# Kernel tuning notes

Hardware: AMD Instinct MI355X
Metric: run time of the kernel (lower is better)

## Reference

```python
import jax, jax.numpy as jnp
import numpy as np

L, D, H, DH, WS, FF = 4, 256, 8, 32, 128, 1024
B, N = 2, 8192
SCALE = DH ** -0.5
EPS = 1e-8


def setup_inputs() -> dict:
    key = jax.random.key(0)
    ks = jax.random.split(key, 24)
    nrm = lambda k, shape, s=0.02: jax.random.normal(k, shape, dtype=jnp.float32) * s
    d = {}
    d["x_real"] = jax.random.normal(ks[0], (B, N, D), dtype=jnp.float32)
    d["x_imag"] = jax.random.normal(ks[1], (B, N, D), dtype=jnp.float32)
    # complex attention projection weights, stored [in, out] (y = x @ W)
    d["Wq_r"] = nrm(ks[2], (L, D, D)); d["Wq_i"] = nrm(ks[3], (L, D, D))
    d["Wk_r"] = nrm(ks[4], (L, D, D)); d["Wk_i"] = nrm(ks[5], (L, D, D))
    d["Wv_r"] = nrm(ks[6], (L, D, D)); d["Wv_i"] = nrm(ks[7], (L, D, D))
    d["Wo_r"] = nrm(ks[8], (L, D, D)); d["Wo_i"] = nrm(ks[9], (L, D, D))
    d["rel_bias"] = nrm(ks[10], (L, 2 * WS + 1))  # std=0.02 per nn.init.normal_
    d["norm1_scale"] = jnp.ones((L, D), jnp.float32)
    d["norm2_scale"] = jnp.ones((L, D), jnp.float32)
    # ComplexFeedForward: real nn.Linear pairs with biases
    d["W1_r"] = nrm(ks[11], (L, D, FF)); d["b1_r"] = jnp.zeros((L, FF), jnp.float32)
    d["W1_i"] = nrm(ks[12], (L, D, FF)); d["b1_i"] = jnp.zeros((L, FF), jnp.float32)
    d["W2_r"] = nrm(ks[13], (L, FF, D)); d["b2_r"] = jnp.zeros((L, D), jnp.float32)
    d["W2_i"] = nrm(ks[14], (L, FF, D)); d["b2_i"] = jnp.zeros((L, D), jnp.float32)
    return d


def _rmsnorm(xr, xi, scale):
    rms = jnp.sqrt(jnp.mean(xr * xr + xi * xi, axis=-1, keepdims=True) + EPS)
    return xr / rms * scale, xi / rms * scale


def _cmm(xr, xi, Wr, Wi):
    # (xr + i xi) @ (Wr + i Wi)
    return xr @ Wr - xi @ Wi, xr @ Wi + xi @ Wr


def _split_heads(t):  # [B,N,H*DH] -> [B,H,NW,WS,DH]
    return t.reshape(B, N // WS, WS, H, DH).transpose(0, 3, 1, 2, 4)


def _attn(xr, xi, Wq_r, Wq_i, Wk_r, Wk_i, Wv_r, Wv_i, Wo_r, Wo_i, rel_bias):
    qr, qi = _cmm(xr, xi, Wq_r, Wq_i)
    kr, ki = _cmm(xr, xi, Wk_r, Wk_i)
    vr, vi = _cmm(xr, xi, Wv_r, Wv_i)
    qr, qi, kr, ki, vr, vi = map(_split_heads, (qr, qi, kr, ki, vr, vi))
    # Re(q . conj(k)) = qr.kr + qi.ki ; windowed (N % WS == 0, no padding)
    dots = (jnp.einsum('bhwid,bhwjd->bhwij', qr, kr)
            + jnp.einsum('bhwid,bhwjd->bhwij', qi, ki)) * SCALE
    idx = (jnp.arange(WS)[None, :] - jnp.arange(WS)[:, None]).clip(-WS, WS) + WS
    dots = dots + rel_bias[idx]  # broadcast over b,h,w
    attn = jax.nn.softmax(dots, axis=-1)  # real-valued probs
    or_ = jnp.einsum('bhwij,bhwjd->bhwid', attn, vr)
    oi_ = jnp.einsum('bhwij,bhwjd->bhwid', attn, vi)
    merge = lambda t: t.transpose(0, 2, 3, 1, 4).reshape(B, N, H * DH)
    or_, oi_ = merge(or_), merge(oi_)
    return _cmm(or_, oi_, Wo_r, Wo_i)


def _ffn(xr, xi, W1_r, b1_r, W1_i, b1_i, W2_r, b2_r, W2_i, b2_i):
    # faithful: w_real(x.real) - w_imag(x.imag) etc., each linear carries its bias
    hr = (xr @ W1_r + b1_r) - (xi @ W1_i + b1_i)
    hi = (xi @ W1_r + b1_r) + (xr @ W1_i + b1_i)
    hr = jax.nn.gelu(hr, approximate=False)
    hi = jax.nn.gelu(hi, approximate=False)
    yr = (hr @ W2_r + b2_r) - (hi @ W2_i + b2_i)
    yi = (hi @ W2_r + b2_r) + (hr @ W2_i + b2_i)
    return yr, yi


def _forward(x_real, x_imag, Wq_r, Wq_i, Wk_r, Wk_i, Wv_r, Wv_i, Wo_r, Wo_i,
             rel_bias, norm1_scale, norm2_scale,
             W1_r, b1_r, W1_i, b1_i, W2_r, b2_r, W2_i, b2_i):
    xr, xi = x_real, x_imag
    for l in range(L):
        nr, ni = _rmsnorm(xr, xi, norm1_scale[l])
        ar, ai = _attn(nr, ni, Wq_r[l], Wq_i[l], Wk_r[l], Wk_i[l],
                       Wv_r[l], Wv_i[l], Wo_r[l], Wo_i[l], rel_bias[l])
        xr, xi = xr + ar, xi + ai
        nr, ni = _rmsnorm(xr, xi, norm2_scale[l])
        fr, fi = _ffn(nr, ni, W1_r[l], b1_r[l], W1_i[l], b1_i[l],
                      W2_r[l], b2_r[l], W2_i[l], b2_i[l])
        xr, xi = xr + fr, xi + fi
    return jnp.stack([xr, xi])  # [2, B, N, D]


def reference(x_real, x_imag, Wq_r, Wq_i, Wk_r, Wk_i, Wv_r, Wv_i, Wo_r, Wo_i,
              rel_bias, norm1_scale, norm2_scale,
              W1_r, b1_r, W1_i, b1_i, W2_r, b2_r, W2_i, b2_i):
    return _forward(x_real, x_imag, Wq_r, Wq_i, Wk_r, Wk_i, Wv_r, Wv_i,
                    Wo_r, Wo_i, rel_bias, norm1_scale, norm2_scale,
                    W1_r, b1_r, W1_i, b1_i, W2_r, b2_r, W2_i, b2_i)
```

## Files before the change

### kernel.cpp

```cpp
#include <hip/hip_runtime.h>
#include <cstdint>


typedef __bf16 bf16x8 __attribute__((ext_vector_type(8)));
typedef float  f32x4  __attribute__((ext_vector_type(4)));

#define M_TOK 16384
#define LDX   512

__device__ __forceinline__ unsigned short f2bf(float f) {
    union { float f; unsigned int u; } v; v.f = f;
    unsigned int r = v.u + 0x7FFFu + ((v.u >> 16) & 1u);
    return (unsigned short)(r >> 16);
}

__device__ __forceinline__ void async16(const void* g, void* l) {
    __builtin_amdgcn_global_load_lds(
        (const __attribute__((address_space(1))) void*)g,
        (__attribute__((address_space(3))) void*)l, 16, 0, 0);
}


__global__ __launch_bounds__(256) void copyin_kernel(const float* __restrict__ xr,
                                                     const float* __restrict__ xi,
                                                     float* __restrict__ X) {
    int idx = blockIdx.x * 256 + threadIdx.x;
    int t = idx >> 7, c4 = idx & 127;
    float4 v = (c4 < 64) ? ((const float4*)xr)[t * 64 + c4]
                         : ((const float4*)xi)[t * 64 + (c4 - 64)];
    ((float4*)X)[idx] = v;
}

__global__ __launch_bounds__(256) void unpack_kernel(const float* __restrict__ X,
                                                     float* __restrict__ out) {
    int idx = blockIdx.x * 256 + threadIdx.x;
    int p = idx >> 20;
    int rem = idx & 1048575;
    int t = rem >> 6, d4 = rem & 63;
    ((float4*)out)[idx] = ((const float4*)X)[t * 128 + p * 64 + d4];
}


__global__ __launch_bounds__(256) void pack_qkv_kernel(
    const float* __restrict__ Wq_r, const float* __restrict__ Wq_i,
    const float* __restrict__ Wk_r, const float* __restrict__ Wk_i,
    const float* __restrict__ Wv_r, const float* __restrict__ Wv_i,
    unsigned short* __restrict__ out) {
    int idx = blockIdx.x * 256 + threadIdx.x;
    int l = idx / 786432;
    int rem = idx - l * 786432;
    int n = rem >> 9, k = rem & 511;
    int blk = n >> 8;
    int no = n & 255, kk = k & 255;
    bool khi = (k >= 256);
    bool imag = (blk & 1);
    const float *Wr, *Wi;
    int proj = blk >> 1;
    if (proj == 0)      { Wr = Wq_r; Wi = Wq_i; }
    else if (proj == 1) { Wr = Wk_r; Wi = Wk_i; }
    else                { Wr = Wv_r; Wi = Wv_i; }
    int wi = l * 65536 + kk * 256 + no;
    float val = !imag ? (khi ? -Wi[wi] : Wr[wi])
                      : (khi ?  Wr[wi] : Wi[wi]);
    out[idx] = f2bf(val);
}

__global__ __launch_bounds__(256) void pack_o_kernel(
    const float* __restrict__ Wo_r, const float* __restrict__ Wo_i,
    unsigned short* __restrict__ out) {
    int idx = blockIdx.x * 256 + threadIdx.x;
    int l = idx >> 18;
    int rem = idx & 262143;
    int n = rem >> 9, k = rem & 511;
    bool imag = (n >= 256);
    int no = n & 255, kk = k & 255;
    bool khi = (k >= 256);
    int wi = l * 65536 + kk * 256 + no;
    float val = !imag ? (khi ? -Wo_i[wi] : Wo_r[wi])
                      : (khi ?  Wo_r[wi] : Wo_i[wi]);
    out[idx] = f2bf(val);
}

__global__ __launch_bounds__(256) void pack_ffn1_kernel(
    const float* __restrict__ W1_r, const float* __restrict__ W1_i,
    unsigned short* __restrict__ out) {
    int idx = blockIdx.x * 256 + threadIdx.x;
    int l = idx >> 20;
    int rem = idx & 1048575;
    int n = rem >> 9, k = rem & 511;
    bool imag = (n >= 1024);
    int no = imag ? n - 1024 : n;
    int kk = k & 255;
    bool khi = (k >= 256);
    int wi = l * 262144 + kk * 1024 + no;
    float val = !imag ? (khi ? -W1_i[wi] : W1_r[wi])
                      : (khi ?  W1_r[wi] : W1_i[wi]);
    out[idx] = f2bf(val);
}

__global__ __launch_bounds__(256) void pack_ffn2_kernel(
    const float* __restrict__ W2_r, const float* __restrict__ W2_i,
    unsigned short* __restrict__ out) {
    int idx = blockIdx.x * 256 + threadIdx.x;
    int l = idx >> 20;
    int rem = idx & 1048575;
    int n = rem >> 11, k = rem & 2047;
    bool imag = (n >= 256);
    int no = n & 255;
    int kk = k & 1023;
    bool khi = (k >= 1024);
    int wi = l * 262144 + kk * 256 + no;
    float val = !imag ? (khi ? -W2_i[wi] : W2_r[wi])
                      : (khi ?  W2_r[wi] : W2_i[wi]);
    out[idx] = f2bf(val);
}

__global__ __launch_bounds__(256) void pack_bias_kernel(
    const float* __restrict__ b1r, const float* __restrict__ b1i,
    const float* __restrict__ b2r, const float* __restrict__ b2i,
    float* __restrict__ B1, float* __restrict__ B2) {
    int idx = blockIdx.x * 256 + threadIdx.x;
    if (idx < 8192) {
        int l = idx >> 11, n = idx & 2047;
        bool imag = (n >= 1024);
        int no = imag ? n - 1024 : n;
        int bi = l * 1024 + no;
        B1[idx] = imag ? (b1r[bi] + b1i[bi]) : (b1r[bi] - b1i[bi]);
    } else {
        int i2 = idx - 8192;
        int l = i2 >> 9, n = i2 & 511;
        bool imag = (n >= 256);
        int no = n & 255;
        int bi = l * 256 + no;
        B2[i2] = imag ? (b2r[bi] + b2i[bi]) : (b2r[bi] - b2i[bi]);
    }
}


__global__ __launch_bounds__(256) void rmsnorm_kernel(const float* __restrict__ X,
                                                      const float* __restrict__ scale,
                                                      unsigned short* __restrict__ out) {
    int row = blockIdx.x * 4 + (threadIdx.x >> 6);
    int lane = threadIdx.x & 63;
    const float4* xrow = (const float4*)(X + (size_t)row * LDX);
    float4 xr = xrow[lane];
    float4 xi = xrow[64 + lane];
    float ss = xr.x * xr.x + xr.y * xr.y + xr.z * xr.z + xr.w * xr.w
             + xi.x * xi.x + xi.y * xi.y + xi.z * xi.z + xi.w * xi.w;
#pragma unroll
    for (int m = 1; m < 64; m <<= 1) ss += __shfl_xor(ss, m);
    float inv = 1.0f / sqrtf(ss * (1.0f / 256.0f) + 1e-8f);
    float4 sc = ((const float4*)scale)[lane];
    ushort4 o0, o1;
    o0.x = f2bf(xr.x * inv * sc.x); o0.y = f2bf(xr.y * inv * sc.y);
    o0.z = f2bf(xr.z * inv * sc.z); o0.w = f2bf(xr.w * inv * sc.w);
    o1.x = f2bf(xi.x * inv * sc.x); o1.y = f2bf(xi.y * inv * sc.y);
    o1.z = f2bf(xi.z * inv * sc.z); o1.w = f2bf(xi.w * inv * sc.w);
    ushort4* orow = (ushort4*)(out + (size_t)row * LDX);
    orow[lane] = o0;
    orow[64 + lane] = o1;
}


template <int MODE>
__global__ __launch_bounds__(256) void gemm_kernel(
    const unsigned short* __restrict__ A, const unsigned short* __restrict__ Bt,
    unsigned short* __restrict__ Obf, const float* __restrict__ bias,
    float* __restrict__ Xres, int K, int N, int nTn) {
    __shared__ __align__(16) char smem[65536];
    const int tid = threadIdx.x;
    const int lane = tid & 63;
    const int wave = tid >> 6;
    const int g = lane >> 4;
    const int rl = lane & 15;
    const int wm = wave >> 1, wn = wave & 1;

    const int nwg = gridDim.x;
    const int qs = nwg >> 3;
    const int xcd = blockIdx.x & 7, pos = blockIdx.x >> 3;
    const int wg = xcd * qs + pos;
    const int tM = wg / nTn, tN = wg - tM * nTn;

    const unsigned short* Abase = A + (size_t)tM * 128 * K;
    const unsigned short* Bbase = Bt + (size_t)tN * 128 * K;
    const int NT = K >> 6;

    auto stage = [&](int t, int buf) {
        char* dA = smem + buf * 32768;
        char* dB = dA + 16384;
        const unsigned short* As = Abase + t * 64;
        const unsigned short* Bs = Bbase + t * 64;
#pragma unroll
        for (int it = 0; it < 4; ++it) {
            int s = it * 256 + tid;
            int r = s >> 3, c = (s & 7) ^ (r & 7);
            async16(As + (size_t)r * K + c * 8, dA + (it * 256 + wave * 64) * 16);
            async16(Bs + (size_t)r * K + c * 8, dB + (it * 256 + wave * 64) * 16);
        }
    };

    f32x4 acc[4][4];
#pragma unroll
    for (int i = 0; i < 4; ++i)
#pragma unroll
        for (int j = 0; j < 4; ++j)
#pragma unroll
            for (int v = 0; v < 4; ++v) acc[i][j][v] = 0.0f;

    stage(0, 0);
    asm volatile("s_waitcnt vmcnt(0)" ::: "memory");
    __syncthreads();

    int cur = 0;
    for (int t = 0; t < NT; ++t) {
        if (t + 1 < NT) stage(t + 1, cur ^ 1);
        char* sA = smem + cur * 32768;
        char* sB = sA + 16384;
#pragma unroll
        for (int ks = 0; ks < 2; ++ks) {
            bf16x8 aF[4], bF[4];
#pragma unroll
            for (int fm = 0; fm < 4; ++fm) {
                int r = wm * 64 + fm * 16 + rl;
                int c = ks * 4 + g;
                aF[fm] = *(const bf16x8*)(sA + r * 128 + ((c ^ (r & 7)) << 4));
            }
#pragma unroll
            for (int fn = 0; fn < 4; ++fn) {
                int r = wn * 64 + fn * 16 + rl;
                int c = ks * 4 + g;
                bF[fn] = *(const bf16x8*)(sB + r * 128 + ((c ^ (r & 7)) << 4));
            }
#pragma unroll
            for (int fm = 0; fm < 4; ++fm)
#pragma unroll
                for (int fn = 0; fn < 4; ++fn)
                    acc[fm][fn] = __builtin_amdgcn_mfma_f32_16x16x32_bf16(
                        aF[fm], bF[fn], acc[fm][fn], 0, 0, 0);
        }
        __syncthreads();
        cur ^= 1;
    }

#pragma unroll
    for (int fm = 0; fm < 4; ++fm)
#pragma unroll
        for (int fn = 0; fn < 4; ++fn)
#pragma unroll
            for (int v = 0; v < 4; ++v) {
                int row = tM * 128 + wm * 64 + fm * 16 + g * 4 + v;
                int col = tN * 128 + wn * 64 + fn * 16 + rl;
                float val = acc[fm][fn][v];
                if (MODE == 0) {
                    Obf[(size_t)row * N + col] = f2bf(val);
                } else if (MODE == 1) {
                    float x = val + bias[col];
                    float ge = 0.5f * x * (1.0f + erff(x * 0.70710678118654752f));
                    Obf[(size_t)row * N + col] = f2bf(ge);
                } else {
                    float x = val + (bias ? bias[col] : 0.0f);
                    Xres[(size_t)row * LDX + col] += x;
                }
            }
}


#define AT_KOFF 16384
#define AT_VOFF 34816
#define AT_ROFF 52224

__global__ __launch_bounds__(256) void attn_kernel(
    const unsigned short* __restrict__ qkv, const float* __restrict__ relb_g,
    unsigned short* __restrict__ attout) {
    __shared__ __align__(16) char smem[53264];
    const int tid = threadIdx.x;
    const int lane = tid & 63;
    const int wq = tid >> 6;
    const int g = lane >> 4;
    const int rl = lane & 15;
    const int w = blockIdx.x, h = blockIdx.y, b = blockIdx.z;
    const int tok0 = b * 8192 + w * 128;
    float* relb = (float*)(smem + AT_ROFF);

    for (int i = tid; i < 257; i += 256) relb[i] = relb_g[i];

#pragma unroll
    for (int it = 0; it < 4; ++it) {
        int s = it * 256 + tid;
        int r = s >> 3;
        int c = (s & 7) ^ (r & 7);
        int colq = (c < 4) ? (h * 32 + c * 8) : (256 + h * 32 + (c - 4) * 8);
        const unsigned short* rowp = qkv + (size_t)(tok0 + r) * 1536;
        *(float4*)(smem + s * 16) = *(const float4*)(rowp + colq);
        *(float4*)(smem + AT_KOFF + s * 16) = *(const float4*)(rowp + colq + 512);
    }
#pragma unroll
    for (int it = 0; it < 4; ++it) {
        int e = it * 256 + tid;
        int j = e >> 3;
        int d0 = (e & 7) * 8;
        int colv = (d0 < 32) ? (1024 + h * 32 + d0) : (1280 + h * 32 + (d0 - 32));
        float4 vv = *(const float4*)(qkv + (size_t)(tok0 + j) * 1536 + colv);
        const unsigned short* u = (const unsigned short*)&vv;
#pragma unroll
        for (int k = 0; k < 8; ++k)
            *(unsigned short*)(smem + AT_VOFF + ((d0 + k) * 136 + j) * 2) = u[k];
    }
    __syncthreads();

    f32x4 accS[2][8];
#pragma unroll
    for (int i = 0; i < 2; ++i)
#pragma unroll
        for (int j = 0; j < 8; ++j)
#pragma unroll
            for (int v = 0; v < 4; ++v) accS[i][j][v] = 0.0f;

#pragma unroll
    for (int ks = 0; ks < 2; ++ks) {
        bf16x8 qf[2], kf[8];
        int c = ks * 4 + g;
#pragma unroll
        for (int fm = 0; fm < 2; ++fm) {
            int r = wq * 32 + fm * 16 + rl;
            qf[fm] = *(const bf16x8*)(smem + r * 128 + ((c ^ (r & 7)) << 4));
        }
#pragma unroll
        for (int fn = 0; fn < 8; ++fn) {
            int r = fn * 16 + rl;
            kf[fn] = *(const bf16x8*)(smem + AT_KOFF + r * 128 + ((c ^ (r & 7)) << 4));
        }
#pragma unroll
        for (int fm = 0; fm < 2; ++fm)
#pragma unroll
            for (int fn = 0; fn < 8; ++fn)
                accS[fm][fn] = __builtin_amdgcn_mfma_f32_16x16x32_bf16(
                    qf[fm], kf[fn], accS[fm][fn], 0, 0, 0);
    }

#pragma unroll
    for (int fm = 0; fm < 2; ++fm)
#pragma unroll
        for (int v = 0; v < 4; ++v) {
            int i = wq * 32 + fm * 16 + g * 4 + v;
            float m = -1e30f;
#pragma unroll
            for (int fn = 0; fn < 8; ++fn) {
                int j = fn * 16 + rl;
                float s = accS[fm][fn][v] * 0.17677669529663687f + relb[j - i + 128];
                accS[fm][fn][v] = s;
                m = fmaxf(m, s);
            }
            m = fmaxf(m, __shfl_xor(m, 1));
            m = fmaxf(m, __shfl_xor(m, 2));
            m = fmaxf(m, __shfl_xor(m, 4));
            m = fmaxf(m, __shfl_xor(m, 8));
            float sum = 0.0f;
#pragma unroll
            for (int fn = 0; fn < 8; ++fn) {
                float p = __expf(accS[fm][fn][v] - m);
                accS[fm][fn][v] = p;
                sum += p;
            }
            sum += __shfl_xor(sum, 1);
            sum += __shfl_xor(sum, 2);
            sum += __shfl_xor(sum, 4);
            sum += __shfl_xor(sum, 8);
            float inv = 1.0f / sum;
#pragma unroll
            for (int fn = 0; fn < 8; ++fn) accS[fm][fn][v] *= inv;
        }

    __syncthreads();

#pragma unroll
    for (int fm = 0; fm < 2; ++fm)
#pragma unroll
        for (int fn = 0; fn < 8; ++fn)
#pragma unroll
            for (int v = 0; v < 4; ++v) {
                int i = wq * 32 + fm * 16 + g * 4 + v;
                int j = fn * 16 + rl;
                ((unsigned short*)smem)[i * 136 + j] = f2bf(accS[fm][fn][v]);
            }
    __syncthreads();

    f32x4 accO[2][4];
#pragma unroll
    for (int i = 0; i < 2; ++i)
#pragma unroll
        for (int j = 0; j < 4; ++j)
#pragma unroll
            for (int v = 0; v < 4; ++v) accO[i][j][v] = 0.0f;

#pragma unroll
    for (int ks = 0; ks < 4; ++ks) {
        bf16x8 pf[2], vf[4];
#pragma unroll
        for (int fm = 0; fm < 2; ++fm) {
            int r = wq * 32 + fm * 16 + rl;
            pf[fm] = *(const bf16x8*)(smem + r * 272 + ks * 64 + g * 16);
        }
#pragma unroll
        for (int fn = 0; fn < 4; ++fn) {
            int n = fn * 16 + rl;
            vf[fn] = *(const bf16x8*)(smem + AT_VOFF + n * 272 + ks * 64 + g * 16);
        }
#pragma unroll
        for (int fm = 0; fm < 2; ++fm)
#pragma unroll
            for (int fn = 0; fn < 4; ++fn)
                accO[fm][fn] = __builtin_amdgcn_mfma_f32_16x16x32_bf16(
                    pf[fm], vf[fn], accO[fm][fn], 0, 0, 0);
    }

#pragma unroll
    for (int fm = 0; fm < 2; ++fm)
#pragma unroll
        for (int fn = 0; fn < 4; ++fn)
#pragma unroll
            for (int v = 0; v < 4; ++v) {
                int i = wq * 32 + fm * 16 + g * 4 + v;
                int dc = fn * 16 + rl;
                int col = (dc < 32) ? (h * 32 + dc) : (256 + h * 32 + (dc - 32));
                attout[(size_t)(tok0 + i) * 512 + col] = f2bf(accO[fm][fn][v]);
            }
}


extern "C" void kernel_launch(void* const* d_in, const int* in_sizes, int n_in,
                              void* d_out, int out_size, void* d_ws, size_t ws_size,
                              hipStream_t stream) {
    const float* x_real = (const float*)d_in[0];
    const float* x_imag = (const float*)d_in[1];
    const float* Wq_r = (const float*)d_in[2];
    const float* Wq_i = (const float*)d_in[3];
    const float* Wk_r = (const float*)d_in[4];
    const float* Wk_i = (const float*)d_in[5];
    const float* Wv_r = (const float*)d_in[6];
    const float* Wv_i = (const float*)d_in[7];
    const float* Wo_r = (const float*)d_in[8];
    const float* Wo_i = (const float*)d_in[9];
    const float* rel_bias = (const float*)d_in[10];
    const float* norm1 = (const float*)d_in[11];
    const float* norm2 = (const float*)d_in[12];
    const float* W1_r = (const float*)d_in[13];
    const float* b1_r = (const float*)d_in[14];
    const float* W1_i = (const float*)d_in[15];
    const float* b1_i = (const float*)d_in[16];
    const float* W2_r = (const float*)d_in[17];
    const float* b2_r = (const float*)d_in[18];
    const float* W2_i = (const float*)d_in[19];
    const float* b2_i = (const float*)d_in[20];

    char* ws = (char*)d_ws;
    float*          X    = (float*)(ws + 0);
    unsigned short* NRM  = (unsigned short*)(ws + 33554432);
    unsigned short* QKVH = (unsigned short*)(ws + 50331648);
    unsigned short* ATTO = (unsigned short*)(ws + 117440512);
    unsigned short* WQKV = (unsigned short*)(ws + 134217728);
    unsigned short* WO   = (unsigned short*)(ws + 140509184);
    unsigned short* W1P  = (unsigned short*)(ws + 142606336);
    unsigned short* W2P  = (unsigned short*)(ws + 150994944);
    float*          B1   = (float*)(ws + 159383552);
    float*          B2   = (float*)(ws + 159416320);

    copyin_kernel<<<8192, 256, 0, stream>>>(x_real, x_imag, X);
    pack_qkv_kernel<<<12288, 256, 0, stream>>>(Wq_r, Wq_i, Wk_r, Wk_i, Wv_r, Wv_i, WQKV);
    pack_o_kernel<<<4096, 256, 0, stream>>>(Wo_r, Wo_i, WO);
    pack_ffn1_kernel<<<16384, 256, 0, stream>>>(W1_r, W1_i, W1P);
    pack_ffn2_kernel<<<16384, 256, 0, stream>>>(W2_r, W2_i, W2P);
    pack_bias_kernel<<<40, 256, 0, stream>>>(b1_r, b1_i, b2_r, b2_i, B1, B2);

    for (int l = 0; l < 4; ++l) {
        rmsnorm_kernel<<<4096, 256, 0, stream>>>(X, norm1 + l * 256, NRM);
        gemm_kernel<0><<<1536, 256, 0, stream>>>(
            NRM, WQKV + (size_t)l * 786432, QKVH, nullptr, nullptr, 512, 1536, 12);
        attn_kernel<<<dim3(64, 8, 2), 256, 0, stream>>>(QKVH, rel_bias + l * 257, ATTO);
        gemm_kernel<2><<<512, 256, 0, stream>>>(
            ATTO, WO + (size_t)l * 262144, nullptr, nullptr, X, 512, 512, 4);
        rmsnorm_kernel<<<4096, 256, 0, stream>>>(X, norm2 + l * 256, NRM);
        gemm_kernel<1><<<2048, 256, 0, stream>>>(
            NRM, W1P + (size_t)l * 1048576, QKVH, B1 + l * 2048, nullptr, 512, 2048, 16);
        gemm_kernel<2><<<512, 256, 0, stream>>>(
            QKVH, W2P + (size_t)l * 1048576, nullptr, B2 + l * 512, X, 2048, 512, 4);
    }
    unpack_kernel<<<8192, 256, 0, stream>>>(X, (float*)d_out);
}
```

Measured before the change: 1.089 ms.

## Enlarge GEMM tiles to 256xBN with 512 threads and deeper async prefetch

Replaces the 128x128, 256-thread GEMM with a templated kernel that uses 256-row by BN-column tiles (BN=256 for FFN1, 128 for the others) and 8 waves. This raises data reuse per LDS load and reduces the number of workgroups. The main loop now keeps two stages of async global-to-LDS loads in flight, using partial vmcnt waits and raw barriers so loads overlap more with MFMA work. The larger LDS footprint (up to 128KB for BN=256) and the smaller grid limit occupancy and can leave some CUs underused.

```diff
diff --git a/kernel.cpp b/kernel.cpp
--- a/kernel.cpp
+++ b/kernel.cpp
@@ -162,94 +162,105 @@
 }
 
 
-template <int MODE>
-__global__ __launch_bounds__(256) void gemm_kernel(
+template <int BN, int MODE>
+__global__ __launch_bounds__(512, 2) void gemm2_kernel(
     const unsigned short* __restrict__ A, const unsigned short* __restrict__ Bt,
     unsigned short* __restrict__ Obf, const float* __restrict__ bias,
     float* __restrict__ Xres, int K, int N, int nTn) {
-    __shared__ __align__(16) char smem[65536];
+    constexpr int FN = BN / 32;
+    constexpr int LB = BN / 64;
+    constexpr int BUFSZ = (256 + BN) * 128;
+    __shared__ __align__(16) char smem[2 * BUFSZ];
     const int tid = threadIdx.x;
     const int lane = tid & 63;
     const int wave = tid >> 6;
-    const int g = lane >> 4;
-    const int rl = lane & 15;
-    const int wm = wave >> 1, wn = wave & 1;
+    const int g = lane >> 4, rl = lane & 15;
+    const int wm = wave & 3, wn = wave >> 2;
 
     const int nwg = gridDim.x;
     const int qs = nwg >> 3;
-    const int xcd = blockIdx.x & 7, pos = blockIdx.x >> 3;
-    const int wg = xcd * qs + pos;
+    const int wg = (blockIdx.x & 7) * qs + (blockIdx.x >> 3);
     const int tM = wg / nTn, tN = wg - tM * nTn;
 
-    const unsigned short* Abase = A + (size_t)tM * 128 * K;
-    const unsigned short* Bbase = Bt + (size_t)tN * 128 * K;
+    const unsigned short* Abase = A + (size_t)tM * 256 * K;
+    const unsigned short* Bbase = Bt + (size_t)tN * BN * K;
     const int NT = K >> 6;
 
     auto stage = [&](int t, int buf) {
-        char* dA = smem + buf * 32768;
-        char* dB = dA + 16384;
+        char* dA = smem + buf * BUFSZ;
+        char* dB = dA + 32768;
         const unsigned short* As = Abase + t * 64;
         const unsigned short* Bs = Bbase + t * 64;
 #pragma unroll
         for (int it = 0; it < 4; ++it) {
-            int s = it * 256 + tid;
+            int s = it * 512 + tid;
             int r = s >> 3, c = (s & 7) ^ (r & 7);
-            async16(As + (size_t)r * K + c * 8, dA + (it * 256 + wave * 64) * 16);
-            async16(Bs + (size_t)r * K + c * 8, dB + (it * 256 + wave * 64) * 16);
+            async16(As + (size_t)r * K + c * 8, dA + (it * 512 + wave * 64) * 16);
+        }
+#pragma unroll
+        for (int it = 0; it < LB; ++it) {
+            int s = it * 512 + tid;
+            int r = s >> 3, c = (s & 7) ^ (r & 7);
+            async16(Bs + (size_t)r * K + c * 8, dB + (it * 512 + wave * 64) * 16);
         }
     };
 
-    f32x4 acc[4][4];
+    f32x4 acc[4][FN];
 #pragma unroll
     for (int i = 0; i < 4; ++i)
 #pragma unroll
-        for (int j = 0; j < 4; ++j)
+        for (int j = 0; j < FN; ++j)
 #pragma unroll
             for (int v = 0; v < 4; ++v) acc[i][j][v] = 0.0f;
 
     stage(0, 0);
-    asm volatile("s_waitcnt vmcnt(0)" ::: "memory");
-    __syncthreads();
+    stage(1, 1);
 
     int cur = 0;
     for (int t = 0; t < NT; ++t) {
-        if (t + 1 < NT) stage(t + 1, cur ^ 1);
-        char* sA = smem + cur * 32768;
-        char* sB = sA + 16384;
+        if (t + 1 < NT) {
+            if constexpr (BN == 256) asm volatile("s_waitcnt vmcnt(8)" ::: "memory");
+            else                     asm volatile("s_waitcnt vmcnt(6)" ::: "memory");
+        } else {
+            asm volatile("s_waitcnt vmcnt(0)" ::: "memory");
+        }
+        __builtin_amdgcn_s_barrier();
+        char* sA = smem + cur * BUFSZ;
+        char* sB = sA + 32768;
 #pragma unroll
         for (int ks = 0; ks < 2; ++ks) {
-            bf16x8 aF[4], bF[4];
+            bf16x8 aF[4], bF[FN];
+            int c = ks * 4 + g;
 #pragma unroll
             for (int fm = 0; fm < 4; ++fm) {
-                int r = wm * 64 + fm * 16 + rl;
-                int c = ks * 4 + g;
-                aF[fm] = *(const bf16x8*)(sA + r * 128 + ((c ^ (r & 7)) << 4));
-            }
-#pragma unroll
-            for (int fn = 0; fn < 4; ++fn) {
-                int r = wn * 64 + fn * 16 + rl;
-                int c = ks * 4 + g;
-                bF[fn] = *(const bf16x8*)(sB + r * 128 + ((c ^ (r & 7)) << 4));
+                int hr = wm * 64 + fm * 16 + rl;
+                aF[fm] = *(const bf16x8*)(sA + hr * 128 + ((c ^ (hr & 7)) << 4));
+            }
+#pragma unroll
+            for (int fn = 0; fn < FN; ++fn) {
+                int hr = wn * (BN / 2) + fn * 16 + rl;
+                bF[fn] = *(const bf16x8*)(sB + hr * 128 + ((c ^ (hr & 7)) << 4));
             }
 #pragma unroll
             for (int fm = 0; fm < 4; ++fm)
 #pragma unroll
-                for (int fn = 0; fn < 4; ++fn)
+                for (int fn = 0; fn < FN; ++fn)
                     acc[fm][fn] = __builtin_amdgcn_mfma_f32_16x16x32_bf16(
                         aF[fm], bF[fn], acc[fm][fn], 0, 0, 0);
         }
-        __syncthreads();
+        __builtin_amdgcn_s_barrier();
+        if (t + 2 < NT) stage(t + 2, cur);
         cur ^= 1;
     }
 
 #pragma unroll
     for (int fm = 0; fm < 4; ++fm)
 #pragma unroll
-        for (int fn = 0; fn < 4; ++fn)
+        for (int fn = 0; fn < FN; ++fn)
 #pragma unroll
             for (int v = 0; v < 4; ++v) {
-                int row = tM * 128 + wm * 64 + fm * 16 + g * 4 + v;
-                int col = tN * 128 + wn * 64 + fn * 16 + rl;
+                int row = tM * 256 + wm * 64 + fm * 16 + g * 4 + v;
+                int col = tN * BN + wn * (BN / 2) + fn * 16 + rl;
                 float val = acc[fm][fn][v];
                 if (MODE == 0) {
                     Obf[(size_t)row * N + col] = f2bf(val);
@@ -474,15 +485,15 @@
 
     for (int l = 0; l < 4; ++l) {
         rmsnorm_kernel<<<4096, 256, 0, stream>>>(X, norm1 + l * 256, NRM);
-        gemm_kernel<0><<<1536, 256, 0, stream>>>(
+        gemm2_kernel<128, 0><<<768, 512, 0, stream>>>(
             NRM, WQKV + (size_t)l * 786432, QKVH, nullptr, nullptr, 512, 1536, 12);
         attn_kernel<<<dim3(64, 8, 2), 256, 0, stream>>>(QKVH, rel_bias + l * 257, ATTO);
-        gemm_kernel<2><<<512, 256, 0, stream>>>(
+        gemm2_kernel<128, 2><<<256, 512, 0, stream>>>(
             ATTO, WO + (size_t)l * 262144, nullptr, nullptr, X, 512, 512, 4);
         rmsnorm_kernel<<<4096, 256, 0, stream>>>(X, norm2 + l * 256, NRM);
-        gemm_kernel<1><<<2048, 256, 0, stream>>>(
-            NRM, W1P + (size_t)l * 1048576, QKVH, B1 + l * 2048, nullptr, 512, 2048, 16);
-        gemm_kernel<2><<<512, 256, 0, stream>>>(
+        gemm2_kernel<256, 1><<<512, 512, 0, stream>>>(
+            NRM, W1P + (size_t)l * 1048576, QKVH, B1 + l * 2048, nullptr, 512, 2048, 8);
+        gemm2_kernel<128, 2><<<256, 512, 0, stream>>>(
             QKVH, W2P + (size_t)l * 1048576, nullptr, B2 + l * 512, X, 2048, 512, 4);
     }
     unpack_kernel<<<8192, 256, 0, stream>>>(X, (float*)d_out);
```

Measured after the change: 1.051 ms. 3.5% less time.

## Keep residual in output buffer as planar layout and deepen GEMM prefetch

Applied to the files above, without the earlier changes.

The residual stream now lives directly in the output buffer in planar real/imag layout, which removes the final unpack kernel and simplifies the copy-in. The GEMM kernel issues two stages ahead and uses partial vmcnt waits with raw barriers, so global-to-LDS loads overlap compute instead of draining each iteration. It also sets launch bounds to request two workgroups per CU. The counted waits depend on the exact number of loads per stage, and the planar residual adds a branch to the epilogue scatter.

```diff
diff --git a/kernel.cpp b/kernel.cpp
--- a/kernel.cpp
+++ b/kernel.cpp
@@ -6,7 +6,7 @@
 typedef float  f32x4  __attribute__((ext_vector_type(4)));
 
 #define M_TOK 16384
-#define LDX   512
+#define PLANE 4194304
 
 __device__ __forceinline__ unsigned short f2bf(float f) {
     union { float f; unsigned int u; } v; v.f = f;
@@ -25,19 +25,9 @@
                                                      const float* __restrict__ xi,
                                                      float* __restrict__ X) {
     int idx = blockIdx.x * 256 + threadIdx.x;
-    int t = idx >> 7, c4 = idx & 127;
-    float4 v = (c4 < 64) ? ((const float4*)xr)[t * 64 + c4]
-                         : ((const float4*)xi)[t * 64 + (c4 - 64)];
-    ((float4*)X)[idx] = v;
-}
-
-__global__ __launch_bounds__(256) void unpack_kernel(const float* __restrict__ X,
-                                                     float* __restrict__ out) {
-    int idx = blockIdx.x * 256 + threadIdx.x;
     int p = idx >> 20;
     int rem = idx & 1048575;
-    int t = rem >> 6, d4 = rem & 63;
-    ((float4*)out)[idx] = ((const float4*)X)[t * 128 + p * 64 + d4];
+    ((float4*)X)[idx] = p ? ((const float4*)xi)[rem] : ((const float4*)xr)[rem];
 }
 
 
@@ -142,9 +132,8 @@
                                                       unsigned short* __restrict__ out) {
     int row = blockIdx.x * 4 + (threadIdx.x >> 6);
     int lane = threadIdx.x & 63;
-    const float4* xrow = (const float4*)(X + (size_t)row * LDX);
-    float4 xr = xrow[lane];
-    float4 xi = xrow[64 + lane];
+    float4 xr = ((const float4*)(X + (size_t)row * 256))[lane];
+    float4 xi = ((const float4*)(X + PLANE + (size_t)row * 256))[lane];
     float ss = xr.x * xr.x + xr.y * xr.y + xr.z * xr.z + xr.w * xr.w
              + xi.x * xi.x + xi.y * xi.y + xi.z * xi.z + xi.w * xi.w;
 #pragma unroll
@@ -156,14 +145,14 @@
     o0.z = f2bf(xr.z * inv * sc.z); o0.w = f2bf(xr.w * inv * sc.w);
     o1.x = f2bf(xi.x * inv * sc.x); o1.y = f2bf(xi.y * inv * sc.y);
     o1.z = f2bf(xi.z * inv * sc.z); o1.w = f2bf(xi.w * inv * sc.w);
-    ushort4* orow = (ushort4*)(out + (size_t)row * LDX);
+    ushort4* orow = (ushort4*)(out + (size_t)row * 512);
     orow[lane] = o0;
     orow[64 + lane] = o1;
 }
 
 
 template <int MODE>
-__global__ __launch_bounds__(256) void gemm_kernel(
+__global__ __launch_bounds__(256, 2) void gemm3_kernel(
     const unsigned short* __restrict__ A, const unsigned short* __restrict__ Bt,
     unsigned short* __restrict__ Obf, const float* __restrict__ bias,
     float* __restrict__ Xres, int K, int N, int nTn) {
@@ -171,14 +160,12 @@
     const int tid = threadIdx.x;
     const int lane = tid & 63;
     const int wave = tid >> 6;
-    const int g = lane >> 4;
-    const int rl = lane & 15;
+    const int g = lane >> 4, rl = lane & 15;
     const int wm = wave >> 1, wn = wave & 1;
 
     const int nwg = gridDim.x;
     const int qs = nwg >> 3;
-    const int xcd = blockIdx.x & 7, pos = blockIdx.x >> 3;
-    const int wg = xcd * qs + pos;
+    const int wg = (blockIdx.x & 7) * qs + (blockIdx.x >> 3);
     const int tM = wg / nTn, tN = wg - tM * nTn;
 
     const unsigned short* Abase = A + (size_t)tM * 128 * K;
@@ -208,28 +195,28 @@
             for (int v = 0; v < 4; ++v) acc[i][j][v] = 0.0f;
 
     stage(0, 0);
-    asm volatile("s_waitcnt vmcnt(0)" ::: "memory");
-    __syncthreads();
+    stage(1, 1);
 
     int cur = 0;
     for (int t = 0; t < NT; ++t) {
-        if (t + 1 < NT) stage(t + 1, cur ^ 1);
+        if (t + 1 < NT) asm volatile("s_waitcnt vmcnt(8)" ::: "memory");
+        else            asm volatile("s_waitcnt vmcnt(0)" ::: "memory");
+        __builtin_amdgcn_s_barrier();
         char* sA = smem + cur * 32768;
         char* sB = sA + 16384;
 #pragma unroll
         for (int ks = 0; ks < 2; ++ks) {
             bf16x8 aF[4], bF[4];
+            int c = ks * 4 + g;
 #pragma unroll
             for (int fm = 0; fm < 4; ++fm) {
-                int r = wm * 64 + fm * 16 + rl;
-                int c = ks * 4 + g;
-                aF[fm] = *(const bf16x8*)(sA + r * 128 + ((c ^ (r & 7)) << 4));
+                int hr = wm * 64 + fm * 16 + rl;
+                aF[fm] = *(const bf16x8*)(sA + hr * 128 + ((c ^ (hr & 7)) << 4));
             }
 #pragma unroll
             for (int fn = 0; fn < 4; ++fn) {
-                int r = wn * 64 + fn * 16 + rl;
-                int c = ks * 4 + g;
-                bF[fn] = *(const bf16x8*)(sB + r * 128 + ((c ^ (r & 7)) << 4));
+                int hr = wn * 64 + fn * 16 + rl;
+                bF[fn] = *(const bf16x8*)(sB + hr * 128 + ((c ^ (hr & 7)) << 4));
             }
 #pragma unroll
             for (int fm = 0; fm < 4; ++fm)
@@ -238,7 +225,8 @@
                     acc[fm][fn] = __builtin_amdgcn_mfma_f32_16x16x32_bf16(
                         aF[fm], bF[fn], acc[fm][fn], 0, 0, 0);
         }
-        __syncthreads();
+        __builtin_amdgcn_s_barrier();
+        if (t + 2 < NT) stage(t + 2, cur);
         cur ^= 1;
     }
 
@@ -259,7 +247,9 @@
                     Obf[(size_t)row * N + col] = f2bf(ge);
                 } else {
                     float x = val + (bias ? bias[col] : 0.0f);
-                    Xres[(size_t)row * LDX + col] += x;
+                    size_t off = (col < 256 ? 0 : (size_t)PLANE)
+                               + (size_t)row * 256 + (col & 255);
+                    Xres[off] += x;
                 }
             }
 }
@@ -453,17 +443,18 @@
     const float* W2_i = (const float*)d_in[19];
     const float* b2_i = (const float*)d_in[20];
 
+    float* X = (float*)d_out;
+
     char* ws = (char*)d_ws;
-    float*          X    = (float*)(ws + 0);
-    unsigned short* NRM  = (unsigned short*)(ws + 33554432);
-    unsigned short* QKVH = (unsigned short*)(ws + 50331648);
-    unsigned short* ATTO = (unsigned short*)(ws + 117440512);
-    unsigned short* WQKV = (unsigned short*)(ws + 134217728);
-    unsigned short* WO   = (unsigned short*)(ws + 140509184);
-    unsigned short* W1P  = (unsigned short*)(ws + 142606336);
-    unsigned short* W2P  = (unsigned short*)(ws + 150994944);
-    float*          B1   = (float*)(ws + 159383552);
-    float*          B2   = (float*)(ws + 159416320);
+    unsigned short* NRM  = (unsigned short*)(ws + 0);
+    unsigned short* QKVH = (unsigned short*)(ws + 16777216);
+    unsigned short* ATTO = (unsigned short*)(ws + 83886080);
+    unsigned short* WQKV = (unsigned short*)(ws + 100663296);
+    unsigned short* WO   = (unsigned short*)(ws + 106954752);
+    unsigned short* W1P  = (unsigned short*)(ws + 109051904);
+    unsigned short* W2P  = (unsigned short*)(ws + 117440512);
+    float*          B1   = (float*)(ws + 125829120);
+    float*          B2   = (float*)(ws + 125861888);
 
     copyin_kernel<<<8192, 256, 0, stream>>>(x_real, x_imag, X);
     pack_qkv_kernel<<<12288, 256, 0, stream>>>(Wq_r, Wq_i, Wk_r, Wk_i, Wv_r, Wv_i, WQKV);
@@ -474,16 +465,15 @@
 
     for (int l = 0; l < 4; ++l) {
         rmsnorm_kernel<<<4096, 256, 0, stream>>>(X, norm1 + l * 256, NRM);
-        gemm_kernel<0><<<1536, 256, 0, stream>>>(
+        gemm3_kernel<0><<<1536, 256, 0, stream>>>(
             NRM, WQKV + (size_t)l * 786432, QKVH, nullptr, nullptr, 512, 1536, 12);
         attn_kernel<<<dim3(64, 8, 2), 256, 0, stream>>>(QKVH, rel_bias + l * 257, ATTO);
-        gemm_kernel<2><<<512, 256, 0, stream>>>(
+        gemm3_kernel<2><<<512, 256, 0, stream>>>(
             ATTO, WO + (size_t)l * 262144, nullptr, nullptr, X, 512, 512, 4);
         rmsnorm_kernel<<<4096, 256, 0, stream>>>(X, norm2 + l * 256, NRM);
-        gemm_kernel<1><<<2048, 256, 0, stream>>>(
+        gemm3_kernel<1><<<2048, 256, 0, stream>>>(
             NRM, W1P + (size_t)l * 1048576, QKVH, B1 + l * 2048, nullptr, 512, 2048, 16);
-        gemm_kernel<2><<<512, 256, 0, stream>>>(
+        gemm3_kernel<2><<<512, 256, 0, stream>>>(
             QKVH, W2P + (size_t)l * 1048576, nullptr, B2 + l * 512, X, 2048, 512, 4);
     }
-    unpack_kernel<<<8192, 256, 0, stream>>>(X, (float*)d_out);
-}
+}
```

Result: faster. 1.038 ms (-4.6%).
